# Kernel optimization log

Hardware: AMD Instinct MI355X
Metric: run time of the kernel (lower is better)

## Reference

```python
import jax, jax.numpy as jnp
import numpy as np

NUM_EMBEDDINGS = 4096
EMBEDDING_DIM = 64
COMMITMENT_COST = 0.25


def setup_inputs() -> dict:
    key = jax.random.key(0)
    kz, kw = jax.random.split(key)
    z = jax.random.normal(kz, (16, 4096, EMBEDDING_DIM), dtype=jnp.float32)
    # torch init: uniform_(-1/num_embeddings, 1/num_embeddings)
    W = jax.random.uniform(kw, (NUM_EMBEDDINGS, EMBEDDING_DIM), dtype=jnp.float32,
                           minval=-1.0 / NUM_EMBEDDINGS, maxval=1.0 / NUM_EMBEDDINGS)
    return {"z": z, "W": W}


def reference(z, W):
    d = W.shape[1]
    zf = z.reshape(-1, d)  # [N, d]
    # squared L2 distances via expansion: ||z||^2 + ||w||^2 - 2 z.w -> [N, K]
    distances = (jnp.sum(zf * zf, axis=1, keepdims=True)
                 + jnp.sum(W * W, axis=1)
                 - 2.0 * jnp.matmul(zf, W.T))
    idx = jnp.argmin(distances, axis=1)          # [N]
    z_q = W[idx].reshape(z.shape)                # gather codebook vectors
    loss = jnp.mean(jnp.square(z - jax.lax.stop_gradient(z_q))) * COMMITMENT_COST
    z_q_out = z + jax.lax.stop_gradient(z_q - z)  # straight-through estimator
    return loss, z_q_out
```

## Files before the change

kernel.cpp:

```cpp
#include <hip/hip_runtime.h>
#include <stdint.h>

typedef int   int4v  __attribute__((ext_vector_type(4)));
typedef int   int8v  __attribute__((ext_vector_type(8)));
typedef float floatx4 __attribute__((ext_vector_type(4)));
typedef float float16v __attribute__((ext_vector_type(16)));

#define BIAS 128.0f

__device__ __forceinline__ void gload_lds16(const void* g, void* l) {
    __builtin_amdgcn_global_load_lds(
        (const __attribute__((address_space(1))) unsigned int*)g,
        (__attribute__((address_space(3))) unsigned int*)l, 16, 0, 0);
}

__global__ void vq_prep(const float* __restrict__ W, unsigned char* __restrict__ Wsw,
                        unsigned int* __restrict__ minidx, float* __restrict__ out0) {
    const int s = blockIdx.x * 256 + threadIdx.x;
    const int T = s >> 7;
    const int q = (s >> 6) & 1;
    const int l = s & 63;
    const int c  = T * 32 + (l & 31);
    const int kb = (l >> 5) * 32 + q * 16;
    const floatx4* wp = (const floatx4*)(W + c * 64 + kb);
    int4v d;
    #pragma unroll
    for (int i = 0; i < 4; ++i) {
        floatx4 f = wp[i];
        int w_ = __builtin_amdgcn_cvt_pk_fp8_f32(f[0] * -4096.0f, f[1] * -4096.0f, 0, false);
        w_ = __builtin_amdgcn_cvt_pk_fp8_f32(f[2] * -4096.0f, f[3] * -4096.0f, w_, true);
        d[i] = w_;
    }
    ((int4v*)Wsw)[s] = d;
    int4v inf = {(int)0xFFFFFFFF, (int)0xFFFFFFFF, (int)0xFFFFFFFF, (int)0xFFFFFFFF};
    ((int4v*)minidx)[s] = inf;
    if (s == 0) *out0 = 0.0f;
}

__launch_bounds__(512)
__attribute__((amdgpu_waves_per_eu(4)))
__global__ void vq_main(const float* __restrict__ z, const unsigned char* __restrict__ Wsw,
                        unsigned int* __restrict__ minidx) {
    __shared__ __align__(16) unsigned char B[65536];

    const int tid  = threadIdx.x;
    const int lane = tid & 63;
    const int wave = tid >> 6;
    const int cg     = blockIdx.x & 3;
    const int rowblk = blockIdx.x >> 2;
    const int l31 = lane & 31;
    const int lh  = lane >> 5;

    #pragma unroll
    for (int i = 0; i < 8; ++i) {
        const int off = (wave * 8 + i) * 1024 + lane * 16;
        gload_lds16(Wsw + cg * 65536 + off, B + off);
    }

    const int rowwave = rowblk * 512 + wave * 64;
    int8v afrag[2];
    #pragma unroll
    for (int mt = 0; mt < 2; ++mt) {
        const floatx4* zp = (const floatx4*)(z + (rowwave + mt * 32 + l31) * 64 + lh * 32);
        int8v fr;
        #pragma unroll
        for (int d = 0; d < 8; ++d) {
            floatx4 v = zp[d];
            int w_ = __builtin_amdgcn_cvt_pk_fp8_f32(v[0], v[1], 0, false);
            w_ = __builtin_amdgcn_cvt_pk_fp8_f32(v[2], v[3], w_, true);
            fr[d] = w_;
        }
        afrag[mt] = fr;
    }

    float16v bias;
    #pragma unroll
    for (int i = 0; i < 16; ++i) bias[i] = BIAS;

    unsigned int minpk[2][16];
    #pragma unroll
    for (int mt = 0; mt < 2; ++mt)
        #pragma unroll
        for (int r = 0; r < 16; ++r) minpk[mt][r] = 0xFFFFFFFFu;

    __syncthreads();

    const unsigned int kk0 = (unsigned int)(cg * 1024 + l31);
    #pragma unroll 2
    for (int t = 0; t < 32; ++t) {
        int4v b0 = *(const int4v*)(B + t * 2048 + lane * 16);
        int4v b1 = *(const int4v*)(B + t * 2048 + 1024 + lane * 16);
        int8v b = {b0[0], b0[1], b0[2], b0[3], b1[0], b1[1], b1[2], b1[3]};
        const unsigned int kk = kk0 + (unsigned int)(t * 32);
        #pragma unroll
        for (int mt = 0; mt < 2; ++mt) {
            float16v acc = __builtin_amdgcn_mfma_scale_f32_32x32x64_f8f6f4(
                afrag[mt], b, bias, 0, 0, 0, 0x7F7F7F7F, 0, 0x7F7F7F7F);
            #pragma unroll
            for (int r = 0; r < 16; ++r) {
                unsigned int p = __float_as_uint(acc[r]) | kk;
                minpk[mt][r] = p < minpk[mt][r] ? p : minpk[mt][r];
            }
        }
    }

    #pragma unroll
    for (int mt = 0; mt < 2; ++mt)
        #pragma unroll
        for (int r = 0; r < 16; ++r) {
            unsigned int v = minpk[mt][r];
            #pragma unroll
            for (int m = 1; m < 32; m <<= 1) {
                unsigned int o = (unsigned int)__shfl_xor((int)v, m, 64);
                v = o < v ? o : v;
            }
            if (l31 == r) {
                const int row = rowwave + mt * 32 + (r & 3) + 8 * (r >> 2) + 4 * lh;
                atomicMin(&minidx[row], v);
            }
        }
}

__launch_bounds__(256)
__global__ void vq_out(const float* __restrict__ z, const float* __restrict__ W,
                       const unsigned int* __restrict__ minidx, float* __restrict__ out) {
    __shared__ float ls[4];
    const int g = blockIdx.x * 256 + threadIdx.x;
    const int row = g >> 2;
    const int seg = g & 3;
    const unsigned int idx = minidx[row] & 0xFFFu;

    const floatx4* wp = (const floatx4*)(W + idx * 64 + seg * 16);
    const floatx4* zp = (const floatx4*)(z + row * 64 + seg * 16);
    floatx4* op = (floatx4*)(out + 1 + row * 64 + seg * 16);
    float loss = 0.0f;
    #pragma unroll
    for (int p2 = 0; p2 < 4; ++p2) {
        floatx4 wv = wp[p2];
        floatx4 zv = zp[p2];
        op[p2] = wv;
        #pragma unroll
        for (int j = 0; j < 4; ++j) {
            float d = zv[j] - wv[j];
            loss = fmaf(d, d, loss);
        }
    }
    #pragma unroll
    for (int m = 1; m < 64; m <<= 1) loss += __shfl_xor(loss, m, 64);
    const int lane = threadIdx.x & 63, wave = threadIdx.x >> 6;
    if (lane == 0) ls[wave] = loss;
    __syncthreads();
    if (threadIdx.x == 0) {
        float t = (ls[0] + ls[1]) + (ls[2] + ls[3]);
        atomicAdd(out, t * (0.25f / 4194304.0f));
    }
}

extern "C" void kernel_launch(void* const* d_in, const int* in_sizes, int n_in,
                              void* d_out, int out_size, void* d_ws, size_t ws_size,
                              hipStream_t stream) {
    (void)in_sizes; (void)n_in; (void)out_size; (void)ws_size;
    const float* z = (const float*)d_in[0];
    const float* W = (const float*)d_in[1];
    unsigned char* Wsw = (unsigned char*)d_ws;
    unsigned int* minidx = (unsigned int*)((char*)d_ws + 262144);
    float* out = (float*)d_out;

    vq_prep<<<64, 256, 0, stream>>>(W, Wsw, minidx, out);
    vq_main<<<512, 512, 0, stream>>>(z, Wsw, minidx);
    vq_out<<<1024, 256, 0, stream>>>(z, W, minidx, out);
}
```

Measured before the change: 118.4 us.

## Split codebook into eight groups with per-group partial argmin buffers instead of atomics

The main kernel now uses 256-thread blocks that each cover 256 rows and one eighth of the codebook (32KB LDS), so there are 2048 blocks instead of 512. Each block writes its packed distance-index minimum to a per-group slot instead of issuing a global atomicMin. The output kernel reduces the eight partials per row, and the prep kernel no longer initialises the min buffer. This trades atomics and larger LDS tiles for more blocks, lower LDS use per block, and an extra eight loads per row in the output kernel. Each block also converts its z rows to fp8 while covering only half as many codes, so total z conversion work doubles.

Result: slower. 129.7 us (+9.5%).

```diff
diff --git a/kernel.cpp b/kernel.cpp
--- a/kernel.cpp
+++ b/kernel.cpp
@@ -15,7 +15,7 @@
 }
 
 __global__ void vq_prep(const float* __restrict__ W, unsigned char* __restrict__ Wsw,
-                        unsigned int* __restrict__ minidx, float* __restrict__ out0) {
+                        float* __restrict__ out0) {
     const int s = blockIdx.x * 256 + threadIdx.x;
     const int T = s >> 7;
     const int q = (s >> 6) & 1;
@@ -32,45 +32,41 @@
         d[i] = w_;
     }
     ((int4v*)Wsw)[s] = d;
-    int4v inf = {(int)0xFFFFFFFF, (int)0xFFFFFFFF, (int)0xFFFFFFFF, (int)0xFFFFFFFF};
-    ((int4v*)minidx)[s] = inf;
     if (s == 0) *out0 = 0.0f;
 }
 
-__launch_bounds__(512)
-__attribute__((amdgpu_waves_per_eu(4)))
+__launch_bounds__(256)
+__attribute__((amdgpu_waves_per_eu(4, 4)))
 __global__ void vq_main(const float* __restrict__ z, const unsigned char* __restrict__ Wsw,
-                        unsigned int* __restrict__ minidx) {
-    __shared__ __align__(16) unsigned char B[65536];
+                        unsigned int* __restrict__ minidx2) {
+    __shared__ __align__(16) unsigned char B[32768];
 
     const int tid  = threadIdx.x;
     const int lane = tid & 63;
     const int wave = tid >> 6;
-    const int cg     = blockIdx.x & 3;
-    const int rowblk = blockIdx.x >> 2;
+    const int cg     = blockIdx.x & 7;
+    const int rowblk = blockIdx.x >> 3;
     const int l31 = lane & 31;
     const int lh  = lane >> 5;
 
     #pragma unroll
     for (int i = 0; i < 8; ++i) {
-        const int off = (wave * 8 + i) * 1024 + lane * 16;
-        gload_lds16(Wsw + cg * 65536 + off, B + off);
+        const int off = wave * 8192 + i * 1024 + lane * 16;
+        gload_lds16(Wsw + cg * 32768 + off, B + off);
     }
 
-    const int rowwave = rowblk * 512 + wave * 64;
+    const int rowwave = rowblk * 256 + wave * 64;
     int8v afrag[2];
     #pragma unroll
     for (int mt = 0; mt < 2; ++mt) {
         const floatx4* zp = (const floatx4*)(z + (rowwave + mt * 32 + l31) * 64 + lh * 32);
-        int8v fr;
         #pragma unroll
         for (int d = 0; d < 8; ++d) {
             floatx4 v = zp[d];
             int w_ = __builtin_amdgcn_cvt_pk_fp8_f32(v[0], v[1], 0, false);
             w_ = __builtin_amdgcn_cvt_pk_fp8_f32(v[2], v[3], w_, true);
-            fr[d] = w_;
+            afrag[mt][d] = w_;
         }
-        afrag[mt] = fr;
     }
 
     float16v bias;
@@ -85,12 +81,12 @@
 
     __syncthreads();
 
-    const unsigned int kk0 = (unsigned int)(cg * 1024 + l31);
-    #pragma unroll 2
-    for (int t = 0; t < 32; ++t) {
-        int4v b0 = *(const int4v*)(B + t * 2048 + lane * 16);
-        int4v b1 = *(const int4v*)(B + t * 2048 + 1024 + lane * 16);
-        int8v b = {b0[0], b0[1], b0[2], b0[3], b1[0], b1[1], b1[2], b1[3]};
+    const unsigned int kk0 = (unsigned int)(cg * 512 + l31);
+    #pragma unroll 1
+    for (int t = 0; t < 16; ++t) {
+        int8v b;
+        *(int4v*)&b       = *(const int4v*)(B + t * 2048 + lane * 16);
+        *((int4v*)&b + 1) = *(const int4v*)(B + t * 2048 + 1024 + lane * 16);
         const unsigned int kk = kk0 + (unsigned int)(t * 32);
         #pragma unroll
         for (int mt = 0; mt < 2; ++mt) {
@@ -104,6 +100,7 @@
         }
     }
 
+    unsigned int* mrow = minidx2 + cg * 65536;
     #pragma unroll
     for (int mt = 0; mt < 2; ++mt)
         #pragma unroll
@@ -116,19 +113,26 @@
             }
             if (l31 == r) {
                 const int row = rowwave + mt * 32 + (r & 3) + 8 * (r >> 2) + 4 * lh;
-                atomicMin(&minidx[row], v);
+                mrow[row] = v;
             }
         }
 }
 
 __launch_bounds__(256)
 __global__ void vq_out(const float* __restrict__ z, const float* __restrict__ W,
-                       const unsigned int* __restrict__ minidx, float* __restrict__ out) {
+                       const unsigned int* __restrict__ minidx2, float* __restrict__ out) {
     __shared__ float ls[4];
     const int g = blockIdx.x * 256 + threadIdx.x;
     const int row = g >> 2;
     const int seg = g & 3;
-    const unsigned int idx = minidx[row] & 0xFFFu;
+
+    unsigned int m0 = minidx2[row];
+    #pragma unroll
+    for (int c = 1; c < 8; ++c) {
+        unsigned int mc = minidx2[c * 65536 + row];
+        m0 = mc < m0 ? mc : m0;
+    }
+    const unsigned int idx = m0 & 0xFFFu;
 
     const floatx4* wp = (const floatx4*)(W + idx * 64 + seg * 16);
     const floatx4* zp = (const floatx4*)(z + row * 64 + seg * 16);
@@ -163,10 +167,10 @@
     const float* z = (const float*)d_in[0];
     const float* W = (const float*)d_in[1];
     unsigned char* Wsw = (unsigned char*)d_ws;
-    unsigned int* minidx = (unsigned int*)((char*)d_ws + 262144);
+    unsigned int* minidx2 = (unsigned int*)((char*)d_ws + 262144);
     float* out = (float*)d_out;
 
-    vq_prep<<<64, 256, 0, stream>>>(W, Wsw, minidx, out);
-    vq_main<<<512, 512, 0, stream>>>(z, Wsw, minidx);
-    vq_out<<<1024, 256, 0, stream>>>(z, W, minidx, out);
+    vq_prep<<<64, 256, 0, stream>>>(W, Wsw, out);
+    vq_main<<<2048, 256, 0, stream>>>(z, Wsw, minidx2);
+    vq_out<<<1024, 256, 0, stream>>>(z, W, minidx2, out);
 }
```
